# Optimization experiments

Hardware: AMD Instinct MI355X
Metric: run time of the kernel (lower is better)

The kernel has to match this reference:

```python
import jax, jax.numpy as jnp
import numpy as np

B, Hs, Ws, C = 1, 48, 48, 768
NH = 12
HD = C // NH          # 64
L = Hs * Ws           # 2304
THETA = 10000.0
SCALE = HD ** -0.5
EPS = 1e-5

# relative coord index table: rel_idx[i, j] = i - j + (H - 1), as in _setup_rel_pos
_REL_IDX = jnp.asarray(np.arange(Hs)[:, None] - np.arange(Ws)[None, :] + (Hs - 1))


def _rope_cos_sin():
    """2D axial RoPE angles (compute_axial_cis): [L, HD//2] cos/sin tables."""
    nf = HD // 4
    freqs = 1.0 / (THETA ** (np.arange(0, HD, 4)[:nf].astype(np.float32) / HD))
    t = np.arange(L, dtype=np.float32)
    tx = t % Hs               # x coord cycles fastest (init_t_xy)
    ty = np.floor(t / Hs)
    ang = np.concatenate([np.outer(tx, freqs), np.outer(ty, freqs)], axis=-1)  # [L, HD//2]
    return jnp.asarray(np.cos(ang)), jnp.asarray(np.sin(ang))


def _layernorm(x, w, b):
    mu = x.mean(-1, keepdims=True)
    var = ((x - mu) ** 2).mean(-1, keepdims=True)
    return (x - mu) * jax.lax.rsqrt(var + EPS) * w + b


def _apply_rope(t, cos, sin):
    # t: [B, NH, L, HD]; view as complex pairs (even=real, odd=imag)
    tr = t.reshape(*t.shape[:-1], HD // 2, 2)
    re, im = tr[..., 0], tr[..., 1]
    out = jnp.stack([re * cos - im * sin, re * sin + im * cos], axis=-1)
    return out.reshape(t.shape)


def setup_inputs() -> dict:
    key = jax.random.key(0)
    ks = jax.random.split(key, 8)
    def rn(k, shape, std=0.02):
        return jax.random.normal(k, shape, dtype=jnp.float32) * std
    return {
        "x": jax.random.normal(ks[0], (B, Hs, Ws, C), dtype=jnp.float32),
        "ln1_w": jnp.ones((C,), jnp.float32),
        "ln1_b": jnp.zeros((C,), jnp.float32),
        "qkv_w": rn(ks[1], (3 * C, C)),
        "qkv_b": jnp.zeros((3 * C,), jnp.float32),
        "rel_pos_h": rn(ks[2], (2 * Hs - 1, HD)),
        "rel_pos_w": rn(ks[3], (2 * Ws - 1, HD)),
        "proj_w": rn(ks[4], (C, C)),
        "proj_b": jnp.zeros((C,), jnp.float32),
        "ln2_w": jnp.ones((C,), jnp.float32),
        "ln2_b": jnp.zeros((C,), jnp.float32),
        "fc1_w": rn(ks[5], (4 * C, C)),
        "fc1_b": jnp.zeros((4 * C,), jnp.float32),
        "fc2_w": rn(ks[6], (C, 4 * C)),
        "fc2_b": jnp.zeros((C,), jnp.float32),
    }


def reference(x, ln1_w, ln1_b, qkv_w, qkv_b, rel_pos_h, rel_pos_w, proj_w, proj_b,
              ln2_w, ln2_b, fc1_w, fc1_b, fc2_w, fc2_b):
    shortcut = x
    h = _layernorm(x, ln1_w, ln1_b)                         # [B,H,W,C]
    qkv = h.reshape(B, L, C) @ qkv_w.T + qkv_b              # [B,L,3C]
    qkv = qkv.reshape(B, L, 3, NH, HD).transpose(2, 0, 3, 1, 4)
    q, k, v = qkv[0], qkv[1], qkv[2]                        # [B,NH,L,HD]

    cos, sin = _rope_cos_sin()
    cos, sin = cos[None, None], sin[None, None]
    q = _apply_rope(q, cos, sin)
    k = _apply_rope(k, cos, sin)

    # Decomposed relative-position bias; math-equivalent to concat_rel_pos
    # (q' = [q*rescale, gathered-rel-vecs], k' = [k, one-hots]) followed by SDPA.
    rq = q.reshape(B, NH, Hs, Ws, HD)
    Rh = rel_pos_h[_REL_IDX]                                # [Hs, Hs(kh), HD]
    Rw = rel_pos_w[_REL_IDX]                                # [Ws, Ws(kw), HD]
    bias_h = jnp.einsum('bnhwc,hkc->bnhwk', rq, Rh)         # over key-row
    bias_w = jnp.einsum('bnhwc,wkc->bnhwk', rq, Rw)         # over key-col

    scores = jnp.einsum('bnqc,bnkc->bnqk', q, k) * SCALE    # [B,NH,L,L]
    scores = scores.reshape(B, NH, Hs, Ws, Hs, Ws) + bias_h[..., :, None] + bias_w[..., None, :]
    attn = jax.nn.softmax(scores.reshape(B, NH, L, L), axis=-1)
    out = jnp.einsum('bnqk,bnkc->bnqc', attn, v)            # [B,NH,L,HD]
    out = out.transpose(0, 2, 1, 3).reshape(B, L, C) @ proj_w.T + proj_b

    x = shortcut + out.reshape(B, Hs, Ws, C)
    h = _layernorm(x, ln2_w, ln2_b)
    h = jax.nn.gelu(h @ fc1_w.T + fc1_b, approximate=False)
    x = x + (h @ fc2_w.T + fc2_b)
    return x
```

## Files before the change

kernel.cpp:

```cpp
#include <hip/hip_runtime.h>
#include <math.h>

#define LTOK 2304
#define CDIM 768
#define NHEAD 12
#define HDIM 64
#define HS 48

typedef short s16x8 __attribute__((ext_vector_type(8)));
typedef float f32x4 __attribute__((ext_vector_type(4)));

__device__ __forceinline__ unsigned short f2b(float f) {
  __bf16 b = (__bf16)f;
  return __builtin_bit_cast(unsigned short, b);
}
__device__ __forceinline__ float b2f(unsigned short u) {
  unsigned int x = ((unsigned int)u) << 16;
  return __builtin_bit_cast(float, x);
}

__device__ __forceinline__ void gld_lds16(void* lds, const void* g) {
  __builtin_amdgcn_global_load_lds(
      (const __attribute__((address_space(1))) unsigned int*)g,
      (__attribute__((address_space(3))) unsigned int*)lds, 16, 0, 0);
}

__global__ __launch_bounds__(256) void f2b4_kernel(const float* __restrict__ a0,
                                                   const float* __restrict__ a1,
                                                   const float* __restrict__ a2,
                                                   const float* __restrict__ a3,
                                                   unsigned short* __restrict__ d0,
                                                   unsigned short* __restrict__ d1,
                                                   unsigned short* __restrict__ d2,
                                                   unsigned short* __restrict__ d3) {
  const int v = blockIdx.x * 256 + threadIdx.x;
  const float* src;
  unsigned short* dst;
  int off;
  if (v < 221184)      { src = a0; dst = d0; off = v; }
  else if (v < 294912) { src = a1; dst = d1; off = v - 221184; }
  else if (v < 589824) { src = a2; dst = d2; off = v - 294912; }
  else                 { src = a3; dst = d3; off = v - 589824; }
  const int i = off * 8;
  float4 v0 = *(const float4*)(src + i);
  float4 v1 = *(const float4*)(src + i + 4);
  alignas(16) unsigned short o[8] = {f2b(v0.x), f2b(v0.y), f2b(v0.z), f2b(v0.w),
                                     f2b(v1.x), f2b(v1.y), f2b(v1.z), f2b(v1.w)};
  *(uint4*)(dst + i) = *(const uint4*)o;
}

__global__ __launch_bounds__(256) void ln_kernel(const float* __restrict__ x,
                                                 const float* __restrict__ w,
                                                 const float* __restrict__ b,
                                                 unsigned short* __restrict__ out) {
  const int row = blockIdx.x;
  const int t = threadIdx.x;
  const float* xr = x + (size_t)row * CDIM;
  float v0 = xr[t], v1 = xr[t + 256], v2 = xr[t + 512];
  float s = v0 + v1 + v2;
  float ss = v0 * v0 + v1 * v1 + v2 * v2;
#pragma unroll
  for (int off = 32; off > 0; off >>= 1) {
    s += __shfl_down(s, off, 64);
    ss += __shfl_down(ss, off, 64);
  }
  __shared__ float rs[4], rss[4];
  if ((t & 63) == 0) { rs[t >> 6] = s; rss[t >> 6] = ss; }
  __syncthreads();
  float S = rs[0] + rs[1] + rs[2] + rs[3];
  float SS = rss[0] + rss[1] + rss[2] + rss[3];
  const float inv_c = 1.0f / (float)CDIM;
  float mu = S * inv_c;
  float var = SS * inv_c - mu * mu;
  float inv = rsqrtf(var + 1e-5f);
  unsigned short* orow = out + (size_t)row * CDIM;
  orow[t]       = f2b((v0 - mu) * inv * w[t]       + b[t]);
  orow[t + 256] = f2b((v1 - mu) * inv * w[t + 256] + b[t + 256]);
  orow[t + 512] = f2b((v2 - mu) * inv * w[t + 512] + b[t + 512]);
}

template <bool GELU, bool RES, bool OUTBF>
__global__ __launch_bounds__(256) void mfma_gemm(const unsigned short* __restrict__ A,
                                                 const unsigned short* __restrict__ B,
                                                 const float* __restrict__ bias,
                                                 const float* __restrict__ res,
                                                 void* __restrict__ Cout,
                                                 int M, int N, int K) {
  __shared__ unsigned short As[2 * 4096];
  __shared__ unsigned short Bs[2 * 4096];
  const int t = threadIdx.x;
  const int lane = t & 63;
  const int w = t >> 6;
  const int wm = w >> 1, wn = w & 1;
  const int bm = blockIdx.y * 128, bn = blockIdx.x * 128;

  f32x4 acc[4][4] = {};

  const int c0 = 2 * w, c1 = 2 * w + 1;
  const int srow = lane >> 2;
  const int skof = (lane & 3) * 8;
  const unsigned short* Abase = A + (size_t)bm * K + skof;
  const unsigned short* Bbase = B + (size_t)bn * K + skof;
  const int lr = lane & 15, lk = (lane >> 4) * 8, lg = lane >> 4;
  const int nk = K >> 5;

  gld_lds16(As + c0 * 512, Abase + (size_t)(c0 * 16 + srow) * K);
  gld_lds16(As + c1 * 512, Abase + (size_t)(c1 * 16 + srow) * K);
  gld_lds16(Bs + c0 * 512, Bbase + (size_t)(c0 * 16 + srow) * K);
  gld_lds16(Bs + c1 * 512, Bbase + (size_t)(c1 * 16 + srow) * K);
  __syncthreads();

#pragma unroll 1
  for (int ks = 0; ks < nk; ++ks) {
    const int off = (ks & 1) * 4096;
    if (ks + 1 < nk) {
      const int noff = 4096 - off;
      const int k1 = (ks + 1) * 32;
      gld_lds16(As + noff + c0 * 512, Abase + (size_t)(c0 * 16 + srow) * K + k1);
      gld_lds16(As + noff + c1 * 512, Abase + (size_t)(c1 * 16 + srow) * K + k1);
      gld_lds16(Bs + noff + c0 * 512, Bbase + (size_t)(c0 * 16 + srow) * K + k1);
      gld_lds16(Bs + noff + c1 * 512, Bbase + (size_t)(c1 * 16 + srow) * K + k1);
    }
    s16x8 a[4], b[4];
#pragma unroll
    for (int m = 0; m < 4; ++m)
      a[m] = *(const s16x8*)&As[off + (wm * 64 + m * 16 + lr) * 32 + lk];
#pragma unroll
    for (int n = 0; n < 4; ++n)
      b[n] = *(const s16x8*)&Bs[off + (wn * 64 + n * 16 + lr) * 32 + lk];
    __builtin_amdgcn_s_setprio(1);
#pragma unroll
    for (int m = 0; m < 4; ++m)
#pragma unroll
      for (int n = 0; n < 4; ++n)
        acc[m][n] = __builtin_amdgcn_mfma_f32_16x16x32_bf16(a[m], b[n], acc[m][n], 0, 0, 0);
    __builtin_amdgcn_s_setprio(0);
    __syncthreads();
  }

#pragma unroll
  for (int n = 0; n < 4; ++n) {
    const int col = bn + wn * 64 + n * 16 + lr;
    const float bc = bias[col];
#pragma unroll
    for (int m = 0; m < 4; ++m) {
#pragma unroll
      for (int j = 0; j < 4; ++j) {
        const int row = bm + wm * 64 + m * 16 + lg * 4 + j;
        float v = acc[m][n][j] + bc;
        if (GELU) v = 0.5f * v * (1.0f + erff(v * 0.70710678118654752f));
        if (RES) v += res[(size_t)row * N + col];
        if (OUTBF) ((unsigned short*)Cout)[(size_t)row * N + col] = f2b(v);
        else       ((float*)Cout)[(size_t)row * N + col] = v;
      }
    }
  }
}

template <bool GELU, bool RES, bool OUTBF>
__global__ __launch_bounds__(256) void gemm64(const unsigned short* __restrict__ A,
                                              const unsigned short* __restrict__ B,
                                              const float* __restrict__ bias,
                                              const float* __restrict__ res,
                                              void* __restrict__ Cout,
                                              int M, int N, int K) {
  __shared__ unsigned short As[2 * 2048];
  __shared__ unsigned short Bs[2 * 4096];
  const int t = threadIdx.x;
  const int lane = t & 63;
  const int w = t >> 6;
  const int wm = w >> 1, wn = w & 1;
  const int bm = blockIdx.y * 64, bn = blockIdx.x * 128;

  f32x4 acc[2][4] = {};

  const int srow = lane >> 2;
  const int skof = (lane & 3) * 8;
  const unsigned short* Abase = A + (size_t)bm * K + skof;
  const unsigned short* Bbase = B + (size_t)bn * K + skof;
  const int lr = lane & 15, lk = (lane >> 4) * 8, lg = lane >> 4;
  const int nk = K >> 5;

  gld_lds16(As + w * 512, Abase + (size_t)(w * 16 + srow) * K);
  gld_lds16(Bs + w * 512, Bbase + (size_t)(w * 16 + srow) * K);
  gld_lds16(Bs + (4 + w) * 512, Bbase + (size_t)((4 + w) * 16 + srow) * K);
  __syncthreads();

#pragma unroll 1
  for (int ks = 0; ks < nk; ++ks) {
    const int offA = (ks & 1) * 2048;
    const int offB = (ks & 1) * 4096;
    if (ks + 1 < nk) {
      const int nA = 2048 - offA, nB = 4096 - offB;
      const int k1 = (ks + 1) * 32;
      gld_lds16(As + nA + w * 512, Abase + (size_t)(w * 16 + srow) * K + k1);
      gld_lds16(Bs + nB + w * 512, Bbase + (size_t)(w * 16 + srow) * K + k1);
      gld_lds16(Bs + nB + (4 + w) * 512, Bbase + (size_t)((4 + w) * 16 + srow) * K + k1);
    }
    s16x8 a[2], b[4];
#pragma unroll
    for (int m = 0; m < 2; ++m)
      a[m] = *(const s16x8*)&As[offA + (wm * 32 + m * 16 + lr) * 32 + lk];
#pragma unroll
    for (int n = 0; n < 4; ++n)
      b[n] = *(const s16x8*)&Bs[offB + (wn * 64 + n * 16 + lr) * 32 + lk];
    __builtin_amdgcn_s_setprio(1);
#pragma unroll
    for (int m = 0; m < 2; ++m)
#pragma unroll
      for (int n = 0; n < 4; ++n)
        acc[m][n] = __builtin_amdgcn_mfma_f32_16x16x32_bf16(a[m], b[n], acc[m][n], 0, 0, 0);
    __builtin_amdgcn_s_setprio(0);
    __syncthreads();
  }

#pragma unroll
  for (int n = 0; n < 4; ++n) {
    const int col = bn + wn * 64 + n * 16 + lr;
    const float bc = bias[col];
#pragma unroll
    for (int m = 0; m < 2; ++m) {
#pragma unroll
      for (int j = 0; j < 4; ++j) {
        const int row = bm + wm * 32 + m * 16 + lg * 4 + j;
        float v = acc[m][n][j] + bc;
        if (GELU) v = 0.5f * v * (1.0f + erff(v * 0.70710678118654752f));
        if (RES) v += res[(size_t)row * N + col];
        if (OUTBF) ((unsigned short*)Cout)[(size_t)row * N + col] = f2b(v);
        else       ((float*)Cout)[(size_t)row * N + col] = v;
      }
    }
  }
}

__global__ __launch_bounds__(256) void rope_cs_kernel(float* __restrict__ cs,
                                                      float* __restrict__ sn) {
  const int idx = blockIdx.x * 256 + threadIdx.x;
  const int l = idx >> 5;
  const int i = idx & 31;
  const int j = i & 15;
  const float f = __expf(-(float)j * 0.57564627324851142f);
  const float coord = (i < 16) ? (float)(l % HS) : (float)(l / HS);
  const float ang = coord * f;
  cs[idx] = cosf(ang);
  sn[idx] = sinf(ang);
}

__global__ __launch_bounds__(256) void prep_kernel(const float* __restrict__ qkv,
                                                   const float* __restrict__ cs,
                                                   const float* __restrict__ sn,
                                                   unsigned short* __restrict__ Qb,
                                                   unsigned short* __restrict__ Kb,
                                                   unsigned short* __restrict__ Vb) {
  __shared__ unsigned short Vs[64 * 72];
  const int t = threadIdx.x;
  const int l0 = blockIdx.x * 64, n = blockIdx.y;
  const int r = t >> 2, c = t & 3;
  const int l = l0 + r;
  const float* base = qkv + (size_t)l * (3 * CDIM) + n * HDIM + c * 16;
#pragma unroll
  for (int pq = 0; pq < 2; ++pq) {
    const float* src = base + pq * CDIM;
    const float qs = pq ? 1.0f : 0.125f;
    alignas(16) unsigned short o[16];
#pragma unroll
    for (int i = 0; i < 4; ++i) {
      float4 v = *(const float4*)(src + i * 4);
      const int pr = c * 8 + i * 2;
      const float c0 = cs[l * 32 + pr],     s0 = sn[l * 32 + pr];
      const float c1 = cs[l * 32 + pr + 1], s1 = sn[l * 32 + pr + 1];
      o[i * 4 + 0] = f2b((v.x * c0 - v.y * s0) * qs);
      o[i * 4 + 1] = f2b((v.x * s0 + v.y * c0) * qs);
      o[i * 4 + 2] = f2b((v.z * c1 - v.w * s1) * qs);
      o[i * 4 + 3] = f2b((v.z * s1 + v.w * c1) * qs);
    }
    unsigned short* dst = (pq ? Kb : Qb) + ((size_t)n * LTOK + l) * HDIM + c * 16;
    *(uint4*)dst = *(const uint4*)o;
    *(uint4*)(dst + 8) = *(const uint4*)(o + 8);
  }
  {
    const float* vsrc = base + 2 * CDIM;
    alignas(16) unsigned short vo[16];
#pragma unroll
    for (int i = 0; i < 4; ++i) {
      float4 v = *(const float4*)(vsrc + i * 4);
      vo[i * 4 + 0] = f2b(v.x); vo[i * 4 + 1] = f2b(v.y);
      vo[i * 4 + 2] = f2b(v.z); vo[i * 4 + 3] = f2b(v.w);
    }
    *(uint4*)&Vs[r * 72 + c * 16] = *(const uint4*)vo;
    *(uint4*)&Vs[r * 72 + c * 16 + 8] = *(const uint4*)(vo + 8);
  }
  __syncthreads();
  {
    const int d = t >> 2, kc16 = (t & 3) * 16;
    alignas(16) unsigned short o[16];
#pragma unroll
    for (int i = 0; i < 16; ++i) o[i] = Vs[(kc16 + i) * 72 + d];
    const int kb = (l0 + kc16) >> 3;
    unsigned short* dst0 = Vb + ((size_t)(n * (LTOK / 8) + kb) * 64 + d) * 8;
    unsigned short* dst1 = Vb + ((size_t)(n * (LTOK / 8) + kb + 1) * 64 + d) * 8;
    *(uint4*)dst0 = *(const uint4*)o;
    *(uint4*)dst1 = *(const uint4*)(o + 8);
  }
}

__global__ __launch_bounds__(256) void attn_mfma(const unsigned short* __restrict__ Qb,
                                                 const unsigned short* __restrict__ Kb,
                                                 const unsigned short* __restrict__ Vb,
                                                 const float* __restrict__ relh,
                                                 const float* __restrict__ relw,
                                                 unsigned short* __restrict__ out) {
  __shared__ __align__(16) unsigned char smem[74752];
  unsigned short* const K_lds = (unsigned short*)(smem);
  unsigned short* const V_lds = (unsigned short*)(smem + 24576);
  unsigned short* const P_lds = (unsigned short*)(smem + 53248);
  float* const bh_t = (float*)(smem + 62464);
  unsigned short* const Q_s = (unsigned short*)(smem + 53248);

  const int t = threadIdx.x;
  const int lane = t & 63, w = t >> 6;
  const int p = lane & 15, g = lane >> 4;
  const int l0 = blockIdx.x * 64, n = blockIdx.y;

  const unsigned short* Khead = Kb + (size_t)n * LTOK * HDIM;
  const unsigned short* Vhead = Vb + (size_t)n * (LTOK / 8) * 64 * 8;

  {
    const int r = t >> 2, c = t & 3;
    const unsigned short* src = Qb + ((size_t)n * LTOK + l0 + r) * HDIM + c * 16;
    uint4 v0 = *(const uint4*)src;
    uint4 v1 = *(const uint4*)(src + 8);
    *(uint4*)&Q_s[r * 72 + c * 16] = v0;
    *(uint4*)&Q_s[r * 72 + c * 16 + 8] = v1;
  }
  __syncthreads();

  const int rowb = lane >> 3;
  const int srcc = (lane & 7) ^ rowb;
  const int kc0 = w, kc1 = w + 4, kc2 = w + 8;

  {
    gld_lds16(K_lds + kc0 * 512, Khead + (size_t)(kc0 * 8 + rowb) * HDIM + srcc * 8);
    gld_lds16(K_lds + kc1 * 512, Khead + (size_t)(kc1 * 8 + rowb) * HDIM + srcc * 8);
    gld_lds16(K_lds + kc2 * 512, Khead + (size_t)(kc2 * 8 + rowb) * HDIM + srcc * 8);
    gld_lds16(V_lds + kc0 * 512, Vhead + kc0 * 512 + lane * 8);
    gld_lds16(V_lds + kc1 * 512, Vhead + kc1 * 512 + lane * 8);
    gld_lds16(V_lds + kc2 * 512, Vhead + kc2 * 512 + lane * 8);
  }
  if (t < 128) *(uint4*)&V_lds[6144 + t * 8] = uint4{0u, 0u, 0u, 0u};
  else         *(uint4*)&V_lds[7168 + 6144 + (t - 128) * 8] = uint4{0u, 0u, 0u, 0u};

  const s16x8 qf0 = *(const s16x8*)&Q_s[(w * 16 + p) * 72 + g * 8];
  const s16x8 qf1 = *(const s16x8*)&Q_s[(w * 16 + p) * 72 + 32 + g * 8];

  const int qh_lane = (l0 + lane) / 48;
#pragma unroll
  for (int i = 0; i < 12; ++i) {
    const int kh = w + 4 * i;
    const float* rrow = relh + (size_t)(qh_lane - kh + 47) * HDIM;
    float acc = 0.f;
#pragma unroll
    for (int c8 = 0; c8 < 8; ++c8) {
      s16x8 qv = *(const s16x8*)&Q_s[lane * 72 + c8 * 8];
      float4 ra = *(const float4*)&rrow[c8 * 8];
      float4 rb = *(const float4*)&rrow[c8 * 8 + 4];
      acc += b2f((unsigned short)qv[0]) * ra.x + b2f((unsigned short)qv[1]) * ra.y +
             b2f((unsigned short)qv[2]) * ra.z + b2f((unsigned short)qv[3]) * ra.w +
             b2f((unsigned short)qv[4]) * rb.x + b2f((unsigned short)qv[5]) * rb.y +
             b2f((unsigned short)qv[6]) * rb.z + b2f((unsigned short)qv[7]) * rb.w;
    }
    bh_t[kh * 64 + lane] = acc * 8.0f;
  }

  float bwreg[12];
  {
    const int qrow = w * 16 + p;
    const int qw_lane = (l0 + qrow) % 48;
#pragma unroll
    for (int mb = 0; mb < 3; ++mb)
#pragma unroll
      for (int jj = 0; jj < 4; ++jj) {
        const int j = 16 * mb + 4 * g + jj;
        const float* rrow = relw + (size_t)(qw_lane - j + 47) * HDIM;
        float acc = 0.f;
#pragma unroll
        for (int c8 = 0; c8 < 8; ++c8) {
          s16x8 qv = *(const s16x8*)&Q_s[qrow * 72 + c8 * 8];
          float4 ra = *(const float4*)&rrow[c8 * 8];
          float4 rb = *(const float4*)&rrow[c8 * 8 + 4];
          acc += b2f((unsigned short)qv[0]) * ra.x + b2f((unsigned short)qv[1]) * ra.y +
                 b2f((unsigned short)qv[2]) * ra.z + b2f((unsigned short)qv[3]) * ra.w +
                 b2f((unsigned short)qv[4]) * rb.x + b2f((unsigned short)qv[5]) * rb.y +
                 b2f((unsigned short)qv[6]) * rb.z + b2f((unsigned short)qv[7]) * rb.w;
        }
        bwreg[mb * 4 + jj] = acc * 8.0f;
      }
  }
  __syncthreads();

  {
    uint2 z = {0u, 0u};
    *(uint2*)&P_lds[(w * 16 + p) * 72 + 48 + 4 * g] = z;
  }

  float lsum = 0.f;
  f32x4 accO[4] = {};
  const int sw0 = g ^ (p & 7);
  const int sw1 = (g + 4) ^ (p & 7);
  unsigned short* const Pw = P_lds + w * 16 * 72;

#pragma unroll 1
  for (int kt = 0; kt < 24; ++kt) {
    const int ko = (kt & 1) * 6144;
    const int vo = (kt & 1) * 7168;
    if (kt < 23) {
      const int nko = 6144 - ko, nvo = 7168 - vo;
      const int kb = (kt + 1) * 96;
      const int vb = (kt + 1) * 12;
      gld_lds16(K_lds + nko + kc0 * 512, Khead + (size_t)(kb + kc0 * 8 + rowb) * HDIM + srcc * 8);
      gld_lds16(K_lds + nko + kc1 * 512, Khead + (size_t)(kb + kc1 * 8 + rowb) * HDIM + srcc * 8);
      gld_lds16(K_lds + nko + kc2 * 512, Khead + (size_t)(kb + kc2 * 8 + rowb) * HDIM + srcc * 8);
      gld_lds16(V_lds + nvo + kc0 * 512, Vhead + (vb + kc0) * 512 + lane * 8);
      gld_lds16(V_lds + nvo + kc1 * 512, Vhead + (vb + kc1) * 512 + lane * 8);
      gld_lds16(V_lds + nvo + kc2 * 512, Vhead + (vb + kc2) * 512 + lane * 8);
    }

#pragma unroll 1
    for (int h = 0; h < 2; ++h) {
      f32x4 st[3] = {};
      __builtin_amdgcn_s_setprio(1);
#pragma unroll
      for (int mb = 0; mb < 3; ++mb) {
        const int krow = ko + (h * 48 + 16 * mb + p) * 64;
        s16x8 kf0 = *(const s16x8*)&K_lds[krow + sw0 * 8];
        s16x8 kf1 = *(const s16x8*)&K_lds[krow + sw1 * 8];
        st[mb] = __builtin_amdgcn_mfma_f32_16x16x32_bf16(kf0, qf0, st[mb], 0, 0, 0);
        st[mb] = __builtin_amdgcn_mfma_f32_16x16x32_bf16(kf1, qf1, st[mb], 0, 0, 0);
      }
      __builtin_amdgcn_s_setprio(0);

      const float bhv = bh_t[(2 * kt + h) * 64 + w * 16 + p] - 8.0f;
      float pv[12], ps = 0.f;
#pragma unroll
      for (int mb = 0; mb < 3; ++mb)
#pragma unroll
        for (int jj = 0; jj < 4; ++jj) {
          const float sv = st[mb][jj] + bhv + bwreg[mb * 4 + jj];
          pv[mb * 4 + jj] = __expf(sv);
          ps += pv[mb * 4 + jj];
        }
      lsum += ps;

#pragma unroll
      for (int mb = 0; mb < 3; ++mb) {
        unsigned int lo = (unsigned int)f2b(pv[mb * 4 + 0]) | ((unsigned int)f2b(pv[mb * 4 + 1]) << 16);
        unsigned int hi = (unsigned int)f2b(pv[mb * 4 + 2]) | ((unsigned int)f2b(pv[mb * 4 + 3]) << 16);
        uint2 val = {lo, hi};
        *(uint2*)&Pw[p * 72 + 16 * mb + 4 * g] = val;
      }

      const s16x8 pf0 = *(const s16x8*)&Pw[p * 72 + g * 8];
      const s16x8 pf1 = *(const s16x8*)&Pw[p * 72 + 32 + g * 8];
      __builtin_amdgcn_s_setprio(1);
#pragma unroll
      for (int db = 0; db < 4; ++db) {
        const int drow = 16 * db + p;
        s16x8 vf0 = *(const s16x8*)&V_lds[vo + ((6 * h + g) * 64 + drow) * 8];
        s16x8 vf1 = *(const s16x8*)&V_lds[vo + ((6 * h + 4 + g) * 64 + drow) * 8];
        accO[db] = __builtin_amdgcn_mfma_f32_16x16x32_bf16(vf0, pf0, accO[db], 0, 0, 0);
        accO[db] = __builtin_amdgcn_mfma_f32_16x16x32_bf16(vf1, pf1, accO[db], 0, 0, 0);
      }
      __builtin_amdgcn_s_setprio(0);
    }

    __syncthreads();
  }

  float ls = lsum + __shfl_xor(lsum, 16, 64);
  ls += __shfl_xor(ls, 32, 64);
  const float inv = 1.0f / ls;
  unsigned short* orow = out + (size_t)(l0 + w * 16 + p) * CDIM + n * HDIM;
#pragma unroll
  for (int db = 0; db < 4; ++db) {
    unsigned int lo = (unsigned int)f2b(accO[db][0] * inv) | ((unsigned int)f2b(accO[db][1] * inv) << 16);
    unsigned int hi = (unsigned int)f2b(accO[db][2] * inv) | ((unsigned int)f2b(accO[db][3] * inv) << 16);
    uint2 val = {lo, hi};
    *(uint2*)&orow[16 * db + 4 * g] = val;
  }
}

extern "C" void kernel_launch(void* const* d_in, const int* in_sizes, int n_in,
                              void* d_out, int out_size, void* d_ws, size_t ws_size,
                              hipStream_t stream) {
  const float* x     = (const float*)d_in[0];
  const float* ln1w  = (const float*)d_in[1];
  const float* ln1b  = (const float*)d_in[2];
  const float* qkvw  = (const float*)d_in[3];
  const float* qkvb  = (const float*)d_in[4];
  const float* relh  = (const float*)d_in[5];
  const float* relw  = (const float*)d_in[6];
  const float* projw = (const float*)d_in[7];
  const float* projb = (const float*)d_in[8];
  const float* ln2w  = (const float*)d_in[9];
  const float* ln2b  = (const float*)d_in[10];
  const float* fc1w  = (const float*)d_in[11];
  const float* fc1b  = (const float*)d_in[12];
  const float* fc2w  = (const float*)d_in[13];
  const float* fc2b  = (const float*)d_in[14];
  float* out = (float*)d_out;
  float* ws = (float*)d_ws;

  float* qkv = ws;
  float* x1  = qkv + (size_t)LTOK * 3 * CDIM;
  float* cs  = x1 + (size_t)LTOK * CDIM;
  float* sn  = cs + (size_t)LTOK * 32;
  unsigned short* h_bf    = (unsigned short*)(sn + (size_t)LTOK * 32);
  unsigned short* attn_bf = h_bf + (size_t)LTOK * CDIM;
  unsigned short* wq      = attn_bf + (size_t)LTOK * CDIM;
  unsigned short* wproj   = wq + (size_t)3 * CDIM * CDIM;
  unsigned short* wfc1    = wproj + (size_t)CDIM * CDIM;
  unsigned short* wfc2    = wfc1 + (size_t)4 * CDIM * CDIM;
  unsigned short* Qb      = (unsigned short*)x1;
  unsigned short* Kb      = Qb + (size_t)NHEAD * LTOK * HDIM;
  unsigned short* Vb      = wq;
  unsigned short* m1_bf   = (unsigned short*)qkv;

  f2b4_kernel<<<3456, 256, 0, stream>>>(qkvw, projw, fc1w, fc2w, wq, wproj, wfc1, wfc2);

  ln_kernel<<<LTOK, 256, 0, stream>>>(x, ln1w, ln1b, h_bf);
  mfma_gemm<false, false, false><<<dim3(18, 18), 256, 0, stream>>>(
      h_bf, wq, qkvb, nullptr, qkv, LTOK, 3 * CDIM, CDIM);
  rope_cs_kernel<<<288, 256, 0, stream>>>(cs, sn);
  prep_kernel<<<dim3(36, 12), 256, 0, stream>>>(qkv, cs, sn, Qb, Kb, Vb);
  attn_mfma<<<dim3(36, 12), 256, 0, stream>>>(Qb, Kb, Vb, relh, relw, attn_bf);
  gemm64<false, true, false><<<dim3(6, 36), 256, 0, stream>>>(
      attn_bf, wproj, projb, x, x1, LTOK, CDIM, CDIM);
  ln_kernel<<<LTOK, 256, 0, stream>>>(x1, ln2w, ln2b, h_bf);
  mfma_gemm<true, false, true><<<dim3(24, 18), 256, 0, stream>>>(
      h_bf, wfc1, fc1b, nullptr, m1_bf, LTOK, 4 * CDIM, CDIM);
  gemm64<false, true, false><<<dim3(6, 36), 256, 0, stream>>>(
      m1_bf, wfc2, fc2b, x1, out, LTOK, CDIM, 4 * CDIM);
}
```

Baseline: 235.9 us.

## Retile GEMMs to 64-row blocks, add K64 GEMM, swizzle attention blocks

The QKV and FC1 GEMMs move from 128x128 tiles to the 64x128 gemm64 kernel, doubling the number of workgroups so the 256 CUs are better filled. A new gemm64k64 kernel stages 64-wide K slices per iteration, halving the barrier count for the proj and FC2 GEMMs, and replaces gemm64 there. The attention launch becomes a 1D grid with a swizzled block-to-(tile, head) mapping, which changes which heads run together across XCDs. Smaller tiles give up some operand reuse, and the larger LDS footprint of the K64 kernel may lower occupancy.

Result: no change. 236.1 us (+0.1%).

```diff
diff --git a/kernel.cpp b/kernel.cpp
--- a/kernel.cpp
+++ b/kernel.cpp
@@ -80,84 +80,6 @@
 }
 
 template <bool GELU, bool RES, bool OUTBF>
-__global__ __launch_bounds__(256) void mfma_gemm(const unsigned short* __restrict__ A,
-                                                 const unsigned short* __restrict__ B,
-                                                 const float* __restrict__ bias,
-                                                 const float* __restrict__ res,
-                                                 void* __restrict__ Cout,
-                                                 int M, int N, int K) {
-  __shared__ unsigned short As[2 * 4096];
-  __shared__ unsigned short Bs[2 * 4096];
-  const int t = threadIdx.x;
-  const int lane = t & 63;
-  const int w = t >> 6;
-  const int wm = w >> 1, wn = w & 1;
-  const int bm = blockIdx.y * 128, bn = blockIdx.x * 128;
-
-  f32x4 acc[4][4] = {};
-
-  const int c0 = 2 * w, c1 = 2 * w + 1;
-  const int srow = lane >> 2;
-  const int skof = (lane & 3) * 8;
-  const unsigned short* Abase = A + (size_t)bm * K + skof;
-  const unsigned short* Bbase = B + (size_t)bn * K + skof;
-  const int lr = lane & 15, lk = (lane >> 4) * 8, lg = lane >> 4;
-  const int nk = K >> 5;
-
-  gld_lds16(As + c0 * 512, Abase + (size_t)(c0 * 16 + srow) * K);
-  gld_lds16(As + c1 * 512, Abase + (size_t)(c1 * 16 + srow) * K);
-  gld_lds16(Bs + c0 * 512, Bbase + (size_t)(c0 * 16 + srow) * K);
-  gld_lds16(Bs + c1 * 512, Bbase + (size_t)(c1 * 16 + srow) * K);
-  __syncthreads();
-
-#pragma unroll 1
-  for (int ks = 0; ks < nk; ++ks) {
-    const int off = (ks & 1) * 4096;
-    if (ks + 1 < nk) {
-      const int noff = 4096 - off;
-      const int k1 = (ks + 1) * 32;
-      gld_lds16(As + noff + c0 * 512, Abase + (size_t)(c0 * 16 + srow) * K + k1);
-      gld_lds16(As + noff + c1 * 512, Abase + (size_t)(c1 * 16 + srow) * K + k1);
-      gld_lds16(Bs + noff + c0 * 512, Bbase + (size_t)(c0 * 16 + srow) * K + k1);
-      gld_lds16(Bs + noff + c1 * 512, Bbase + (size_t)(c1 * 16 + srow) * K + k1);
-    }
-    s16x8 a[4], b[4];
-#pragma unroll
-    for (int m = 0; m < 4; ++m)
-      a[m] = *(const s16x8*)&As[off + (wm * 64 + m * 16 + lr) * 32 + lk];
-#pragma unroll
-    for (int n = 0; n < 4; ++n)
-      b[n] = *(const s16x8*)&Bs[off + (wn * 64 + n * 16 + lr) * 32 + lk];
-    __builtin_amdgcn_s_setprio(1);
-#pragma unroll
-    for (int m = 0; m < 4; ++m)
-#pragma unroll
-      for (int n = 0; n < 4; ++n)
-        acc[m][n] = __builtin_amdgcn_mfma_f32_16x16x32_bf16(a[m], b[n], acc[m][n], 0, 0, 0);
-    __builtin_amdgcn_s_setprio(0);
-    __syncthreads();
-  }
-
-#pragma unroll
-  for (int n = 0; n < 4; ++n) {
-    const int col = bn + wn * 64 + n * 16 + lr;
-    const float bc = bias[col];
-#pragma unroll
-    for (int m = 0; m < 4; ++m) {
-#pragma unroll
-      for (int j = 0; j < 4; ++j) {
-        const int row = bm + wm * 64 + m * 16 + lg * 4 + j;
-        float v = acc[m][n][j] + bc;
-        if (GELU) v = 0.5f * v * (1.0f + erff(v * 0.70710678118654752f));
-        if (RES) v += res[(size_t)row * N + col];
-        if (OUTBF) ((unsigned short*)Cout)[(size_t)row * N + col] = f2b(v);
-        else       ((float*)Cout)[(size_t)row * N + col] = v;
-      }
-    }
-  }
-}
-
-template <bool GELU, bool RES, bool OUTBF>
 __global__ __launch_bounds__(256) void gemm64(const unsigned short* __restrict__ A,
                                               const unsigned short* __restrict__ B,
                                               const float* __restrict__ bias,
@@ -233,6 +155,93 @@
   }
 }
 
+template <bool GELU, bool RES, bool OUTBF>
+__global__ __launch_bounds__(256) void gemm64k64(const unsigned short* __restrict__ A,
+                                                 const unsigned short* __restrict__ B,
+                                                 const float* __restrict__ bias,
+                                                 const float* __restrict__ res,
+                                                 void* __restrict__ Cout,
+                                                 int M, int N, int K) {
+  __shared__ unsigned short As[2 * 4096];
+  __shared__ unsigned short Bs[2 * 8192];
+  const int t = threadIdx.x;
+  const int lane = t & 63;
+  const int w = t >> 6;
+  const int wm = w >> 1, wn = w & 1;
+  const int bm = blockIdx.y * 64, bn = blockIdx.x * 128;
+
+  f32x4 acc[2][4] = {};
+
+  const int srow = lane >> 3;
+  const int skof = (lane & 7) * 8;
+  const unsigned short* Abase = A + (size_t)bm * K + skof;
+  const unsigned short* Bbase = B + (size_t)bn * K + skof;
+  const int ca0 = 2 * w, ca1 = 2 * w + 1;
+  const int cb0 = 4 * w, cb1 = 4 * w + 1, cb2 = 4 * w + 2, cb3 = 4 * w + 3;
+  const int lr = lane & 15, lk = (lane >> 4) * 8, lg = lane >> 4;
+  const int nk = K >> 6;
+
+  gld_lds16(As + ca0 * 512, Abase + (size_t)(ca0 * 8 + srow) * K);
+  gld_lds16(As + ca1 * 512, Abase + (size_t)(ca1 * 8 + srow) * K);
+  gld_lds16(Bs + cb0 * 512, Bbase + (size_t)(cb0 * 8 + srow) * K);
+  gld_lds16(Bs + cb1 * 512, Bbase + (size_t)(cb1 * 8 + srow) * K);
+  gld_lds16(Bs + cb2 * 512, Bbase + (size_t)(cb2 * 8 + srow) * K);
+  gld_lds16(Bs + cb3 * 512, Bbase + (size_t)(cb3 * 8 + srow) * K);
+  __syncthreads();
+
+#pragma unroll 1
+  for (int ks = 0; ks < nk; ++ks) {
+    const int offA = (ks & 1) * 4096;
+    const int offB = (ks & 1) * 8192;
+    if (ks + 1 < nk) {
+      const int nA = 4096 - offA, nB = 8192 - offB;
+      const int k1 = (ks + 1) * 64;
+      gld_lds16(As + nA + ca0 * 512, Abase + (size_t)(ca0 * 8 + srow) * K + k1);
+      gld_lds16(As + nA + ca1 * 512, Abase + (size_t)(ca1 * 8 + srow) * K + k1);
+      gld_lds16(Bs + nB + cb0 * 512, Bbase + (size_t)(cb0 * 8 + srow) * K + k1);
+      gld_lds16(Bs + nB + cb1 * 512, Bbase + (size_t)(cb1 * 8 + srow) * K + k1);
+      gld_lds16(Bs + nB + cb2 * 512, Bbase + (size_t)(cb2 * 8 + srow) * K + k1);
+      gld_lds16(Bs + nB + cb3 * 512, Bbase + (size_t)(cb3 * 8 + srow) * K + k1);
+    }
+#pragma unroll
+    for (int kk = 0; kk < 2; ++kk) {
+      s16x8 a[2], b[4];
+#pragma unroll
+      for (int m = 0; m < 2; ++m)
+        a[m] = *(const s16x8*)&As[offA + (wm * 32 + m * 16 + lr) * 64 + kk * 32 + lk];
+#pragma unroll
+      for (int n = 0; n < 4; ++n)
+        b[n] = *(const s16x8*)&Bs[offB + (wn * 64 + n * 16 + lr) * 64 + kk * 32 + lk];
+      __builtin_amdgcn_s_setprio(1);
+#pragma unroll
+      for (int m = 0; m < 2; ++m)
+#pragma unroll
+        for (int n = 0; n < 4; ++n)
+          acc[m][n] = __builtin_amdgcn_mfma_f32_16x16x32_bf16(a[m], b[n], acc[m][n], 0, 0, 0);
+      __builtin_amdgcn_s_setprio(0);
+    }
+    __syncthreads();
+  }
+
+#pragma unroll
+  for (int n = 0; n < 4; ++n) {
+    const int col = bn + wn * 64 + n * 16 + lr;
+    const float bc = bias[col];
+#pragma unroll
+    for (int m = 0; m < 2; ++m) {
+#pragma unroll
+      for (int j = 0; j < 4; ++j) {
+        const int row = bm + wm * 32 + m * 16 + lg * 4 + j;
+        float v = acc[m][n][j] + bc;
+        if (GELU) v = 0.5f * v * (1.0f + erff(v * 0.70710678118654752f));
+        if (RES) v += res[(size_t)row * N + col];
+        if (OUTBF) ((unsigned short*)Cout)[(size_t)row * N + col] = f2b(v);
+        else       ((float*)Cout)[(size_t)row * N + col] = v;
+      }
+    }
+  }
+}
+
 __global__ __launch_bounds__(256) void rope_cs_kernel(float* __restrict__ cs,
                                                       float* __restrict__ sn) {
   const int idx = blockIdx.x * 256 + threadIdx.x;
@@ -320,7 +329,9 @@
   const int t = threadIdx.x;
   const int lane = t & 63, w = t >> 6;
   const int p = lane & 15, g = lane >> 4;
-  const int l0 = blockIdx.x * 64, n = blockIdx.y;
+  const int bid = blockIdx.x;
+  const int swz = (bid & 7) * 54 + (bid >> 3);
+  const int l0 = (swz % 36) * 64, n = swz / 36;
 
   const unsigned short* Khead = Kb + (size_t)n * LTOK * HDIM;
   const unsigned short* Vhead = Vb + (size_t)n * (LTOK / 8) * 64 * 8;
@@ -528,16 +539,16 @@
   f2b4_kernel<<<3456, 256, 0, stream>>>(qkvw, projw, fc1w, fc2w, wq, wproj, wfc1, wfc2);
 
   ln_kernel<<<LTOK, 256, 0, stream>>>(x, ln1w, ln1b, h_bf);
-  mfma_gemm<false, false, false><<<dim3(18, 18), 256, 0, stream>>>(
+  gemm64<false, false, false><<<dim3(18, 36), 256, 0, stream>>>(
       h_bf, wq, qkvb, nullptr, qkv, LTOK, 3 * CDIM, CDIM);
   rope_cs_kernel<<<288, 256, 0, stream>>>(cs, sn);
   prep_kernel<<<dim3(36, 12), 256, 0, stream>>>(qkv, cs, sn, Qb, Kb, Vb);
-  attn_mfma<<<dim3(36, 12), 256, 0, stream>>>(Qb, Kb, Vb, relh, relw, attn_bf);
-  gemm64<false, true, false><<<dim3(6, 36), 256, 0, stream>>>(
+  attn_mfma<<<432, 256, 0, stream>>>(Qb, Kb, Vb, relh, relw, attn_bf);
+  gemm64k64<false, true, false><<<dim3(6, 36), 256, 0, stream>>>(
       attn_bf, wproj, projb, x, x1, LTOK, CDIM, CDIM);
   ln_kernel<<<LTOK, 256, 0, stream>>>(x1, ln2w, ln2b, h_bf);
-  mfma_gemm<true, false, true><<<dim3(24, 18), 256, 0, stream>>>(
+  gemm64<true, false, true><<<dim3(24, 36), 256, 0, stream>>>(
       h_bf, wfc1, fc1b, nullptr, m1_bf, LTOK, 4 * CDIM, CDIM);
-  gemm64<false, true, false><<<dim3(6, 36), 256, 0, stream>>>(
+  gemm64k64<false, true, false><<<dim3(6, 36), 256, 0, stream>>>(
       m1_bf, wfc2, fc2b, x1, out, LTOK, CDIM, 4 * CDIM);
 }
```
